# Performance work log

Measured on AMD Instinct MI355X. Metric: run time of the kernel, lower is better.

The kernel has to match this reference:

```python
import jax, jax.numpy as jnp
import numpy as np
import math

B, S, D, H, DFF = 4, 1024, 1024, 16, 4096
DK = D // H
EPS = 1e-5


def setup_inputs() -> dict:
    key = jax.random.key(0)
    ks = jax.random.split(key, 16)
    sc = 0.02
    inp = {
        "x": jax.random.normal(ks[0], (B, S, D), jnp.float32),
        "Wq": jax.random.normal(ks[1], (D, D), jnp.float32) * sc,
        "bq": jnp.zeros((D,), jnp.float32),
        "Wk": jax.random.normal(ks[2], (D, D), jnp.float32) * sc,
        "bk": jnp.zeros((D,), jnp.float32),
        "Wv": jax.random.normal(ks[3], (D, D), jnp.float32) * sc,
        "bv": jnp.zeros((D,), jnp.float32),
        "Wo": jax.random.normal(ks[4], (D, D), jnp.float32) * sc,
        "bo": jnp.zeros((D,), jnp.float32),
        "W1": jax.random.normal(ks[5], (D, DFF), jnp.float32) * sc,
        "b1": jnp.zeros((DFF,), jnp.float32),
        "W2": jax.random.normal(ks[6], (DFF, D), jnp.float32) * sc,
        "b2": jnp.zeros((D,), jnp.float32),
        "g1": jnp.ones((D,), jnp.float32),
        "be1": jnp.zeros((D,), jnp.float32),
        "g2": jnp.ones((D,), jnp.float32),
        "be2": jnp.zeros((D,), jnp.float32),
    }
    return inp


def _layernorm(x, g, b):
    mu = jnp.mean(x, axis=-1, keepdims=True)
    var = jnp.mean(jnp.square(x - mu), axis=-1, keepdims=True)
    return (x - mu) * jax.lax.rsqrt(var + EPS) * g + b


def reference(x, Wq, bq, Wk, bk, Wv, bv, Wo, bo, W1, b1, W2, b2, g1, be1, g2, be2):
    # multi-head self-attention (dropout = identity, eval mode)
    q = (x @ Wq + bq).reshape(B, S, H, DK).transpose(0, 2, 1, 3)  # [B,H,S,DK]
    k = (x @ Wk + bk).reshape(B, S, H, DK).transpose(0, 2, 1, 3)
    v = (x @ Wv + bv).reshape(B, S, H, DK).transpose(0, 2, 1, 3)
    scores = jnp.einsum("bhqd,bhkd->bhqk", q, k) / math.sqrt(DK)
    attn_weights = jax.nn.softmax(scores, axis=-1)
    ctx = jnp.einsum("bhqk,bhkd->bhqd", attn_weights, v)
    ctx = ctx.transpose(0, 2, 1, 3).reshape(B, S, D)
    attn_out = ctx @ Wo + bo
    x = _layernorm(x + attn_out, g1, be1)
    ff = jax.nn.relu(x @ W1 + b1) @ W2 + b2
    x = _layernorm(x + ff, g2, be2)
    return x, attn_weights
```

## Files before the change

### kernel.cpp

```cpp
#include <hip/hip_runtime.h>

typedef unsigned short u16;
typedef __attribute__((ext_vector_type(8))) short bf16x8;
typedef __attribute__((ext_vector_type(4))) float f32x4;

__device__ __forceinline__ u16 f2b(float f) {
  unsigned u = __float_as_uint(f);
  u += 0x7fffu + ((u >> 16) & 1u);
  return (u16)(u >> 16);
}
__device__ __forceinline__ float b2f(u16 v) {
  return __uint_as_float((unsigned)v << 16);
}

__device__ __forceinline__ void gload16(const u16* g, u16* l) {
  __builtin_amdgcn_global_load_lds((__attribute__((address_space(1))) void*)(g),
                                   (__attribute__((address_space(3))) void*)(l), 16, 0, 0);
}

__global__ __launch_bounds__(256) void cast_k(const float* __restrict__ s,
                                              u16* __restrict__ d, int n4) {
  int i = blockIdx.x * 256 + threadIdx.x;
  if (i >= n4) return;
  float4 v = *(const float4*)(s + (size_t)i * 4);
  ushort4 o = make_ushort4(f2b(v.x), f2b(v.y), f2b(v.z), f2b(v.w));
  *(ushort4*)(d + (size_t)i * 4) = o;
}

__global__ __launch_bounds__(256) void transpose_k(const float* __restrict__ src,
                                                   u16* __restrict__ dst,
                                                   int ldsrc, int lddst) {
  __shared__ float t[32][33];
  int c0 = blockIdx.x * 32, r0 = blockIdx.y * 32;
  int tx = threadIdx.x, ty = threadIdx.y;
#pragma unroll
  for (int i = 0; i < 4; ++i)
    t[ty + i * 8][tx] = src[(size_t)(r0 + ty + i * 8) * ldsrc + c0 + tx];
  __syncthreads();
#pragma unroll
  for (int i = 0; i < 4; ++i)
    dst[(size_t)(c0 + ty + i * 8) * lddst + r0 + tx] = f2b(t[tx][ty + i * 8]);
}

__global__ __launch_bounds__(256) void transpose_v_k(const u16* __restrict__ qkv,
                                                     u16* __restrict__ vt) {
  __shared__ u16 t[32][33];
  int z = blockIdx.z;
  int b = z >> 4, h = z & 15;
  int s0 = blockIdx.x * 32, d0 = blockIdx.y * 32;
  int tx = threadIdx.x, ty = threadIdx.y;
  const u16* src = qkv + (size_t)(b * 1024) * 3072 + 2048 + h * 64;
  u16* dst = vt + (size_t)z * 65536;
#pragma unroll
  for (int i = 0; i < 4; ++i)
    t[ty + i * 8][tx] = src[(size_t)(s0 + ty + i * 8) * 3072 + d0 + tx];
  __syncthreads();
#pragma unroll
  for (int i = 0; i < 4; ++i)
    dst[(size_t)(d0 + ty + i * 8) * 1024 + s0 + tx] = t[tx][ty + i * 8];
}

template <int BN, int BIAS, int RELU, int EXPE, int RSCALE, int SB16, int SF32>
__global__ __launch_bounds__(256) void gemm_k(
    const u16* __restrict__ Ab, long aHi, long aLo, int lda,
    const u16* __restrict__ Bt, long bHi, long bLo, int ldb,
    float* __restrict__ Cf, u16* __restrict__ Cb,
    long cHi, long cLo, int ldc,
    const float* __restrict__ bias, const float* __restrict__ rs,
    int K, int ZD) {
  constexpr int NT = BN / 32;
  constexpr int CB = (BN * 64 * 2) / 1024;
  __shared__ __align__(128) u16 As[128 * 64];
  __shared__ __align__(128) u16 Bs[BN * 64];

  const int tid = threadIdx.x;
  const int lane = tid & 63;
  const int wave = tid >> 6;
  const int waveM = wave >> 1, waveN = wave & 1;
  const int quad = lane >> 4, l16 = lane & 15;

  const int zb = blockIdx.z / ZD, zr = blockIdx.z % ZD;
  const long aOff = zb * aHi + zr * aLo;
  const long bOff = zb * bHi + zr * bLo;
  const long cOff = zb * cHi + zr * cLo;

  const int row0 = blockIdx.y * 128;
  const int col0 = blockIdx.x * BN;

  const int lr = lane >> 3;
  const int lc = (lane & 7) * 8;

  f32x4 acc[4][NT] = {};

  for (int k0 = 0; k0 < K; k0 += 64) {
    const u16* Ag = Ab + aOff + (long)row0 * lda + k0;
    const u16* Bg = Bt + bOff + (long)col0 * ldb + k0;
#pragma unroll
    for (int c = 0; c < 4; ++c) {
      int ch = c * 4 + wave;
      gload16(Ag + (long)(ch * 8 + lr) * lda + lc, &As[ch * 512]);
    }
#pragma unroll
    for (int c = 0; c < CB / 4; ++c) {
      int ch = c * 4 + wave;
      gload16(Bg + (long)(ch * 8 + lr) * ldb + lc, &Bs[ch * 512]);
    }
    __syncthreads();

    bf16x8 af[4][2], bfr[NT][2];
#pragma unroll
    for (int mi = 0; mi < 4; ++mi)
#pragma unroll
      for (int ks = 0; ks < 2; ++ks)
        af[mi][ks] = *(const bf16x8*)&As[(waveM * 64 + mi * 16 + l16) * 64 + ks * 32 + quad * 8];
#pragma unroll
    for (int ni = 0; ni < NT; ++ni)
#pragma unroll
      for (int ks = 0; ks < 2; ++ks)
        bfr[ni][ks] = *(const bf16x8*)&Bs[(waveN * (BN / 2) + ni * 16 + l16) * 64 + ks * 32 + quad * 8];
#pragma unroll
    for (int ks = 0; ks < 2; ++ks)
#pragma unroll
      for (int mi = 0; mi < 4; ++mi)
#pragma unroll
        for (int ni = 0; ni < NT; ++ni)
          acc[mi][ni] = __builtin_amdgcn_mfma_f32_16x16x32_bf16(af[mi][ks], bfr[ni][ks], acc[mi][ni], 0, 0, 0);
    __syncthreads();
  }

#pragma unroll
  for (int ni = 0; ni < NT; ++ni) {
    int col = col0 + waveN * (BN / 2) + ni * 16 + l16;
    float bv = BIAS ? bias[col] : 0.f;
#pragma unroll
    for (int mi = 0; mi < 4; ++mi) {
#pragma unroll
      for (int r = 0; r < 4; ++r) {
        int row = row0 + waveM * 64 + mi * 16 + quad * 4 + r;
        float v = acc[mi][ni][r] + bv;
        if (RELU) v = fmaxf(v, 0.f);
        if (EXPE) v = __expf(v * 0.125f);
        if (RSCALE) v *= rs[(long)blockIdx.z * 1024 + row];
        long idx = cOff + (long)row * ldc + col;
        if (SF32) Cf[idx] = v;
        if (SB16) Cb[idx] = f2b(v);
      }
    }
  }
}

__global__ __launch_bounds__(256) void norm_k(const u16* __restrict__ e,
                                              float* __restrict__ w,
                                              float* __restrict__ inv) {
  long row = blockIdx.x;
  int tid = threadIdx.x;
  ushort4 ev = *(const ushort4*)(e + row * 1024 + tid * 4);
  float4 v;
  v.x = b2f(ev.x); v.y = b2f(ev.y); v.z = b2f(ev.z); v.w = b2f(ev.w);
  float s = v.x + v.y + v.z + v.w;
#pragma unroll
  for (int d = 32; d > 0; d >>= 1) s += __shfl_xor(s, d);
  __shared__ float red[4];
  if ((tid & 63) == 0) red[tid >> 6] = s;
  __syncthreads();
  s = red[0] + red[1] + red[2] + red[3];
  float r = 1.f / s;
  float4 o = make_float4(v.x * r, v.y * r, v.z * r, v.w * r);
  *(float4*)(w + row * 1024 + tid * 4) = o;
  if (tid == 0) inv[row] = r;
}

template <int WB16>
__global__ __launch_bounds__(256) void add_ln_k(const float* __restrict__ xp,
                                                const float* __restrict__ yp,
                                                const float* __restrict__ g,
                                                const float* __restrict__ bta,
                                                float* __restrict__ of,
                                                u16* __restrict__ ob) {
  long row = blockIdx.x;
  int tid = threadIdx.x;
  const float4 xv = *(const float4*)(xp + row * 1024 + tid * 4);
  const float4 yv = *(const float4*)(yp + row * 1024 + tid * 4);
  float4 v = make_float4(xv.x + yv.x, xv.y + yv.y, xv.z + yv.z, xv.w + yv.w);
  float s1 = v.x + v.y + v.z + v.w;
  float s2 = v.x * v.x + v.y * v.y + v.z * v.z + v.w * v.w;
#pragma unroll
  for (int d = 32; d > 0; d >>= 1) {
    s1 += __shfl_xor(s1, d);
    s2 += __shfl_xor(s2, d);
  }
  __shared__ float r1[4], r2[4];
  if ((tid & 63) == 0) { r1[tid >> 6] = s1; r2[tid >> 6] = s2; }
  __syncthreads();
  s1 = r1[0] + r1[1] + r1[2] + r1[3];
  s2 = r2[0] + r2[1] + r2[2] + r2[3];
  float mu = s1 * (1.f / 1024.f);
  float var = s2 * (1.f / 1024.f) - mu * mu;
  float rs = rsqrtf(var + 1e-5f);
  float4 gv = *(const float4*)(g + tid * 4);
  float4 bv = *(const float4*)(bta + tid * 4);
  float4 o;
  o.x = (v.x - mu) * rs * gv.x + bv.x;
  o.y = (v.y - mu) * rs * gv.y + bv.y;
  o.z = (v.z - mu) * rs * gv.z + bv.z;
  o.w = (v.w - mu) * rs * gv.w + bv.w;
  *(float4*)(of + row * 1024 + tid * 4) = o;
  if (WB16) {
    ushort4 ov = make_ushort4(f2b(o.x), f2b(o.y), f2b(o.z), f2b(o.w));
    *(ushort4*)(ob + row * 1024 + tid * 4) = ov;
  }
}

extern "C" void kernel_launch(void* const* d_in, const int* in_sizes, int n_in,
                              void* d_out, int out_size, void* d_ws, size_t ws_size,
                              hipStream_t stream) {
  const float* x   = (const float*)d_in[0];
  const float* Wq  = (const float*)d_in[1];
  const float* bq  = (const float*)d_in[2];
  const float* Wk  = (const float*)d_in[3];
  const float* bk  = (const float*)d_in[4];
  const float* Wv  = (const float*)d_in[5];
  const float* bv  = (const float*)d_in[6];
  const float* Wo  = (const float*)d_in[7];
  const float* bo  = (const float*)d_in[8];
  const float* W1  = (const float*)d_in[9];
  const float* b1  = (const float*)d_in[10];
  const float* W2  = (const float*)d_in[11];
  const float* b2  = (const float*)d_in[12];
  const float* g1  = (const float*)d_in[13];
  const float* be1 = (const float*)d_in[14];
  const float* g2  = (const float*)d_in[15];
  const float* be2 = (const float*)d_in[16];

  float* out = (float*)d_out;
  float* attn = out + 4194304LL;

  char* w = (char*)d_ws;
  size_t off = 0;
  auto alloc = [&](size_t bytes) {
    void* p = w + off;
    off = (off + bytes + 255) & ~(size_t)255;
    return p;
  };
  u16* xb        = (u16*)alloc(8388608);
  u16* Wqkvt     = (u16*)alloc(6291456);
  u16* Wot       = (u16*)alloc(2097152);
  u16* W1t       = (u16*)alloc(8388608);
  u16* W2t       = (u16*)alloc(8388608);
  float* bqkv    = (float*)alloc(12288);
  u16* qkvb      = (u16*)alloc(25165824);
  u16* vtb       = (u16*)alloc(8388608);
  u16* expb      = (u16*)alloc(134217728);
  float* inv     = (float*)alloc(262144);
  u16* ctxb      = (u16*)alloc(8388608);
  float* attn_o  = (float*)alloc(16777216);
  float* x1      = (float*)alloc(16777216);
  u16* x1b       = (u16*)alloc(8388608);
  u16* ff1b      = (u16*)alloc(33554432);
  float* ff2     = (float*)alloc(16777216);
  (void)ws_size; (void)in_sizes; (void)n_in; (void)out_size;

  dim3 tb(32, 8);
  cast_k<<<4096, 256, 0, stream>>>(x, xb, 1048576);
  transpose_k<<<dim3(32, 32), tb, 0, stream>>>(Wq, Wqkvt,           1024, 1024);
  transpose_k<<<dim3(32, 32), tb, 0, stream>>>(Wk, Wqkvt + 1048576, 1024, 1024);
  transpose_k<<<dim3(32, 32), tb, 0, stream>>>(Wv, Wqkvt + 2097152, 1024, 1024);
  transpose_k<<<dim3(32, 32), tb, 0, stream>>>(Wo, Wot, 1024, 1024);
  transpose_k<<<dim3(128, 32), tb, 0, stream>>>(W1, W1t, 4096, 1024);
  transpose_k<<<dim3(32, 128), tb, 0, stream>>>(W2, W2t, 1024, 4096);
  hipMemcpyAsync(bqkv,        bq, 4096, hipMemcpyDeviceToDevice, stream);
  hipMemcpyAsync(bqkv + 1024, bk, 4096, hipMemcpyDeviceToDevice, stream);
  hipMemcpyAsync(bqkv + 2048, bv, 4096, hipMemcpyDeviceToDevice, stream);

  gemm_k<128, 1, 0, 0, 0, 1, 0><<<dim3(24, 32, 1), 256, 0, stream>>>(
      xb, 0, 0, 1024, Wqkvt, 0, 0, 1024,
      nullptr, qkvb, 0, 0, 3072, bqkv, nullptr, 1024, 1);

  transpose_v_k<<<dim3(32, 2, 64), tb, 0, stream>>>(qkvb, vtb);

  gemm_k<128, 0, 0, 1, 0, 1, 0><<<dim3(8, 8, 64), 256, 0, stream>>>(
      qkvb, 3145728L, 64, 3072,
      qkvb + 1024, 3145728L, 64, 3072,
      nullptr, expb, 16777216L, 1048576L, 1024, nullptr, nullptr, 64, 16);

  norm_k<<<65536, 256, 0, stream>>>(expb, attn, inv);

  gemm_k<64, 0, 0, 0, 1, 1, 0><<<dim3(1, 8, 64), 256, 0, stream>>>(
      expb, 16777216L, 1048576L, 1024,
      vtb, 1048576L, 65536L, 1024,
      nullptr, ctxb, 1048576L, 64, 1024, nullptr, inv, 1024, 16);

  gemm_k<128, 1, 0, 0, 0, 0, 1><<<dim3(8, 32, 1), 256, 0, stream>>>(
      ctxb, 0, 0, 1024, Wot, 0, 0, 1024,
      attn_o, nullptr, 0, 0, 1024, bo, nullptr, 1024, 1);

  add_ln_k<1><<<4096, 256, 0, stream>>>(x, attn_o, g1, be1, x1, x1b);

  gemm_k<128, 1, 1, 0, 0, 1, 0><<<dim3(32, 32, 1), 256, 0, stream>>>(
      x1b, 0, 0, 1024, W1t, 0, 0, 1024,
      nullptr, ff1b, 0, 0, 4096, b1, nullptr, 1024, 1);

  gemm_k<128, 1, 0, 0, 0, 0, 1><<<dim3(8, 32, 1), 256, 0, stream>>>(
      ff1b, 0, 0, 4096, W2t, 0, 0, 4096,
      ff2, nullptr, 0, 0, 1024, b2, nullptr, 4096, 1);

  add_ln_k<0><<<4096, 256, 0, stream>>>(x1, ff2, g2, be2, out, nullptr);
}
```

Measured before the change: 753.9 us.

## Fuse score GEMM with softmax, fold residual into GEMM epilogue, merge weight transposes

Replaces the score GEMM, separate bf16 exp write, and row-normalization kernel with one kernel. It computes QK^T per 64-row tile, keeps exp values in registers, reduces the row sums and writes normalized fp32 attention plus bf16 probabilities. This removes a full re-read of the 128MB exp buffer. The residual add moves into the Wo and W2 GEMM epilogues, and those GEMMs switch to BN=64 with more blocks. The four square weight transposes merge into one launch, and the bias memcpys are replaced by multi-pointer bias selection. The fused softmax holds 128 packed registers per thread, which limits occupancy and risks spills.

```diff
diff --git a/kernel.cpp b/kernel.cpp
--- a/kernel.cpp
+++ b/kernel.cpp
@@ -40,6 +40,27 @@
 #pragma unroll
   for (int i = 0; i < 4; ++i)
     dst[(size_t)(c0 + ty + i * 8) * lddst + r0 + tx] = f2b(t[tx][ty + i * 8]);
+}
+
+__global__ __launch_bounds__(256) void transpose4_k(const float* __restrict__ Wq,
+                                                    const float* __restrict__ Wk,
+                                                    const float* __restrict__ Wv,
+                                                    const float* __restrict__ Wo,
+                                                    u16* __restrict__ Wqkvt,
+                                                    u16* __restrict__ Wot) {
+  __shared__ float t[32][33];
+  int z = blockIdx.z;
+  const float* src = z == 0 ? Wq : z == 1 ? Wk : z == 2 ? Wv : Wo;
+  u16* dst = z < 3 ? Wqkvt + (size_t)z * 1048576 : Wot;
+  int c0 = blockIdx.x * 32, r0 = blockIdx.y * 32;
+  int tx = threadIdx.x, ty = threadIdx.y;
+#pragma unroll
+  for (int i = 0; i < 4; ++i)
+    t[ty + i * 8][tx] = src[(size_t)(r0 + ty + i * 8) * 1024 + c0 + tx];
+  __syncthreads();
+#pragma unroll
+  for (int i = 0; i < 4; ++i)
+    dst[(size_t)(c0 + ty + i * 8) * 1024 + r0 + tx] = f2b(t[tx][ty + i * 8]);
 }
 
 __global__ __launch_bounds__(256) void transpose_v_k(const u16* __restrict__ qkv,
@@ -57,16 +78,17 @@
   __syncthreads();
 #pragma unroll
   for (int i = 0; i < 4; ++i)
-    dst[(size_t)(d0 + ty + i * 8) * 1024 + s0 + tx] = t[tx][ty + i * 8];
-}
-
-template <int BN, int BIAS, int RELU, int EXPE, int RSCALE, int SB16, int SF32>
+    dst[(size_t)(d0 + i * 8 + ty) * 1024 + s0 + tx] = t[tx][ty + i * 8];
+}
+
+template <int BN, int BIAS, int RELU, int SB16, int SF32, int RESID>
 __global__ __launch_bounds__(256) void gemm_k(
     const u16* __restrict__ Ab, long aHi, long aLo, int lda,
     const u16* __restrict__ Bt, long bHi, long bLo, int ldb,
     float* __restrict__ Cf, u16* __restrict__ Cb,
     long cHi, long cLo, int ldc,
-    const float* __restrict__ bias, const float* __restrict__ rs,
+    const float* __restrict__ bias, const float* __restrict__ biasB,
+    const float* __restrict__ biasC, const float* __restrict__ resid,
     int K, int ZD) {
   constexpr int NT = BN / 32;
   constexpr int CB = (BN * 64 * 2) / 1024;
@@ -131,7 +153,9 @@
 #pragma unroll
   for (int ni = 0; ni < NT; ++ni) {
     int col = col0 + waveN * (BN / 2) + ni * 16 + l16;
-    float bv = BIAS ? bias[col] : 0.f;
+    float bv = 0.f;
+    if (BIAS == 1) bv = bias[col];
+    if (BIAS == 3) bv = col < 1024 ? bias[col] : (col < 2048 ? biasB[col - 1024] : biasC[col - 2048]);
 #pragma unroll
     for (int mi = 0; mi < 4; ++mi) {
 #pragma unroll
@@ -139,9 +163,8 @@
         int row = row0 + waveM * 64 + mi * 16 + quad * 4 + r;
         float v = acc[mi][ni][r] + bv;
         if (RELU) v = fmaxf(v, 0.f);
-        if (EXPE) v = __expf(v * 0.125f);
-        if (RSCALE) v *= rs[(long)blockIdx.z * 1024 + row];
         long idx = cOff + (long)row * ldc + col;
+        if (RESID) v += resid[idx];
         if (SF32) Cf[idx] = v;
         if (SB16) Cb[idx] = f2b(v);
       }
@@ -149,28 +172,87 @@
   }
 }
 
-__global__ __launch_bounds__(256) void norm_k(const u16* __restrict__ e,
-                                              float* __restrict__ w,
-                                              float* __restrict__ inv) {
-  long row = blockIdx.x;
-  int tid = threadIdx.x;
-  ushort4 ev = *(const ushort4*)(e + row * 1024 + tid * 4);
-  float4 v;
-  v.x = b2f(ev.x); v.y = b2f(ev.y); v.z = b2f(ev.z); v.w = b2f(ev.w);
-  float s = v.x + v.y + v.z + v.w;
-#pragma unroll
-  for (int d = 32; d > 0; d >>= 1) s += __shfl_xor(s, d);
-  __shared__ float red[4];
-  if ((tid & 63) == 0) red[tid >> 6] = s;
-  __syncthreads();
-  s = red[0] + red[1] + red[2] + red[3];
-  float r = 1.f / s;
-  float4 o = make_float4(v.x * r, v.y * r, v.z * r, v.w * r);
-  *(float4*)(w + row * 1024 + tid * 4) = o;
-  if (tid == 0) inv[row] = r;
-}
-
-template <int WB16>
+__global__ __launch_bounds__(256) void score_softmax_k(const u16* __restrict__ qkvb,
+                                                       float* __restrict__ attn,
+                                                       u16* __restrict__ expb) {
+  __shared__ __align__(128) u16 Bs[256 * 64];
+  const int tid = threadIdx.x;
+  const int lane = tid & 63;
+  const int w = tid >> 6;
+  const int quad = lane >> 4, l16 = lane & 15;
+  const int lr = lane >> 3, lc = (lane & 7) * 8;
+
+  const int z = blockIdx.y;
+  const int b = z >> 4, h = z & 15;
+  const u16* Q  = qkvb + (long)b * 3145728 + h * 64;
+  const u16* Kt = qkvb + (long)b * 3145728 + 1024 + h * 64;
+
+  const int qrow = blockIdx.x * 64 + w * 16 + l16;
+  bf16x8 af[2];
+  af[0] = *(const bf16x8*)&Q[(long)qrow * 3072 + quad * 8];
+  af[1] = *(const bf16x8*)&Q[(long)qrow * 3072 + 32 + quad * 8];
+
+  unsigned p[4][32];
+  float rowpart[4] = {0.f, 0.f, 0.f, 0.f};
+
+#pragma unroll 4
+  for (int nc = 0; nc < 4; ++nc) {
+#pragma unroll
+    for (int c = 0; c < 8; ++c) {
+      int ch = c * 4 + w;
+      gload16(Kt + (long)(nc * 256 + ch * 8 + lr) * 3072 + lc, &Bs[ch * 512]);
+    }
+    __syncthreads();
+#pragma unroll
+    for (int ni = 0; ni < 16; ++ni) {
+      bf16x8 b0 = *(const bf16x8*)&Bs[(ni * 16 + l16) * 64 + quad * 8];
+      bf16x8 b1 = *(const bf16x8*)&Bs[(ni * 16 + l16) * 64 + 32 + quad * 8];
+      f32x4 acc = {};
+      acc = __builtin_amdgcn_mfma_f32_16x16x32_bf16(af[0], b0, acc, 0, 0, 0);
+      acc = __builtin_amdgcn_mfma_f32_16x16x32_bf16(af[1], b1, acc, 0, 0, 0);
+      float e0 = __expf(acc[0] * 0.125f);
+      float e1 = __expf(acc[1] * 0.125f);
+      float e2 = __expf(acc[2] * 0.125f);
+      float e3 = __expf(acc[3] * 0.125f);
+      rowpart[0] += e0; rowpart[1] += e1; rowpart[2] += e2; rowpart[3] += e3;
+      p[nc][ni * 2]     = (unsigned)f2b(e0) | ((unsigned)f2b(e1) << 16);
+      p[nc][ni * 2 + 1] = (unsigned)f2b(e2) | ((unsigned)f2b(e3) << 16);
+    }
+    __syncthreads();
+  }
+
+#pragma unroll
+  for (int d = 1; d < 16; d <<= 1) {
+#pragma unroll
+    for (int r = 0; r < 4; ++r) rowpart[r] += __shfl_xor(rowpart[r], d);
+  }
+  float inv0 = 1.f / rowpart[0], inv1 = 1.f / rowpart[1];
+  float inv2 = 1.f / rowpart[2], inv3 = 1.f / rowpart[3];
+
+  const long rbase = (long)z * 1048576 + (long)(blockIdx.x * 64 + w * 16 + quad * 4) * 1024;
+#pragma unroll 4
+  for (int nc = 0; nc < 4; ++nc) {
+#pragma unroll
+    for (int ni = 0; ni < 16; ++ni) {
+      int col = nc * 256 + ni * 16 + l16;
+      unsigned w0 = p[nc][ni * 2], w1 = p[nc][ni * 2 + 1];
+      float e0 = b2f((u16)(w0 & 0xffff)) * inv0;
+      float e1 = b2f((u16)(w0 >> 16)) * inv1;
+      float e2 = b2f((u16)(w1 & 0xffff)) * inv2;
+      float e3 = b2f((u16)(w1 >> 16)) * inv3;
+      attn[rbase + col] = e0;
+      attn[rbase + 1024 + col] = e1;
+      attn[rbase + 2048 + col] = e2;
+      attn[rbase + 3072 + col] = e3;
+      expb[rbase + col] = f2b(e0);
+      expb[rbase + 1024 + col] = f2b(e1);
+      expb[rbase + 2048 + col] = f2b(e2);
+      expb[rbase + 3072 + col] = f2b(e3);
+    }
+  }
+}
+
+template <int WB16, int ADD>
 __global__ __launch_bounds__(256) void add_ln_k(const float* __restrict__ xp,
                                                 const float* __restrict__ yp,
                                                 const float* __restrict__ g,
@@ -179,9 +261,11 @@
                                                 u16* __restrict__ ob) {
   long row = blockIdx.x;
   int tid = threadIdx.x;
-  const float4 xv = *(const float4*)(xp + row * 1024 + tid * 4);
-  const float4 yv = *(const float4*)(yp + row * 1024 + tid * 4);
-  float4 v = make_float4(xv.x + yv.x, xv.y + yv.y, xv.z + yv.z, xv.w + yv.w);
+  float4 v = *(const float4*)(xp + row * 1024 + tid * 4);
+  if (ADD) {
+    const float4 yv = *(const float4*)(yp + row * 1024 + tid * 4);
+    v.x += yv.x; v.y += yv.y; v.z += yv.z; v.w += yv.w;
+  }
   float s1 = v.x + v.y + v.z + v.w;
   float s2 = v.x * v.x + v.y * v.y + v.z * v.z + v.w * v.w;
 #pragma unroll
@@ -247,11 +331,9 @@
   u16* Wot       = (u16*)alloc(2097152);
   u16* W1t       = (u16*)alloc(8388608);
   u16* W2t       = (u16*)alloc(8388608);
-  float* bqkv    = (float*)alloc(12288);
   u16* qkvb      = (u16*)alloc(25165824);
   u16* vtb       = (u16*)alloc(8388608);
   u16* expb      = (u16*)alloc(134217728);
-  float* inv     = (float*)alloc(262144);
   u16* ctxb      = (u16*)alloc(8388608);
   float* attn_o  = (float*)alloc(16777216);
   float* x1      = (float*)alloc(16777216);
@@ -262,47 +344,36 @@
 
   dim3 tb(32, 8);
   cast_k<<<4096, 256, 0, stream>>>(x, xb, 1048576);
-  transpose_k<<<dim3(32, 32), tb, 0, stream>>>(Wq, Wqkvt,           1024, 1024);
-  transpose_k<<<dim3(32, 32), tb, 0, stream>>>(Wk, Wqkvt + 1048576, 1024, 1024);
-  transpose_k<<<dim3(32, 32), tb, 0, stream>>>(Wv, Wqkvt + 2097152, 1024, 1024);
-  transpose_k<<<dim3(32, 32), tb, 0, stream>>>(Wo, Wot, 1024, 1024);
+  transpose4_k<<<dim3(32, 32, 4), tb, 0, stream>>>(Wq, Wk, Wv, Wo, Wqkvt, Wot);
   transpose_k<<<dim3(128, 32), tb, 0, stream>>>(W1, W1t, 4096, 1024);
   transpose_k<<<dim3(32, 128), tb, 0, stream>>>(W2, W2t, 1024, 4096);
-  hipMemcpyAsync(bqkv,        bq, 4096, hipMemcpyDeviceToDevice, stream);
-  hipMemcpyAsync(bqkv + 1024, bk, 4096, hipMemcpyDeviceToDevice, stream);
-  hipMemcpyAsync(bqkv + 2048, bv, 4096, hipMemcpyDeviceToDevice, stream);
-
-  gemm_k<128, 1, 0, 0, 0, 1, 0><<<dim3(24, 32, 1), 256, 0, stream>>>(
+
+  gemm_k<128, 3, 0, 1, 0, 0><<<dim3(24, 32, 1), 256, 0, stream>>>(
       xb, 0, 0, 1024, Wqkvt, 0, 0, 1024,
-      nullptr, qkvb, 0, 0, 3072, bqkv, nullptr, 1024, 1);
+      nullptr, qkvb, 0, 0, 3072, bq, bk, bv, nullptr, 1024, 1);
 
   transpose_v_k<<<dim3(32, 2, 64), tb, 0, stream>>>(qkvb, vtb);
 
-  gemm_k<128, 0, 0, 1, 0, 1, 0><<<dim3(8, 8, 64), 256, 0, stream>>>(
-      qkvb, 3145728L, 64, 3072,
-      qkvb + 1024, 3145728L, 64, 3072,
-      nullptr, expb, 16777216L, 1048576L, 1024, nullptr, nullptr, 64, 16);
-
-  norm_k<<<65536, 256, 0, stream>>>(expb, attn, inv);
-
-  gemm_k<64, 0, 0, 0, 1, 1, 0><<<dim3(1, 8, 64), 256, 0, stream>>>(
+  score_softmax_k<<<dim3(16, 64), 256, 0, stream>>>(qkvb, attn, expb);
+
+  gemm_k<64, 0, 0, 1, 0, 0><<<dim3(1, 8, 64), 256, 0, stream>>>(
       expb, 16777216L, 1048576L, 1024,
       vtb, 1048576L, 65536L, 1024,
-      nullptr, ctxb, 1048576L, 64, 1024, nullptr, inv, 1024, 16);
-
-  gemm_k<128, 1, 0, 0, 0, 0, 1><<<dim3(8, 32, 1), 256, 0, stream>>>(
+      nullptr, ctxb, 1048576L, 64, 1024, nullptr, nullptr, nullptr, nullptr, 1024, 16);
+
+  gemm_k<64, 1, 0, 0, 1, 1><<<dim3(16, 32, 1), 256, 0, stream>>>(
       ctxb, 0, 0, 1024, Wot, 0, 0, 1024,
-      attn_o, nullptr, 0, 0, 1024, bo, nullptr, 1024, 1);
-
-  add_ln_k<1><<<4096, 256, 0, stream>>>(x, attn_o, g1, be1, x1, x1b);
-
-  gemm_k<128, 1, 1, 0, 0, 1, 0><<<dim3(32, 32, 1), 256, 0, stream>>>(
+      attn_o, nullptr, 0, 0, 1024, bo, nullptr, nullptr, x, 1024, 1);
+
+  add_ln_k<1, 0><<<4096, 256, 0, stream>>>(attn_o, nullptr, g1, be1, x1, x1b);
+
+  gemm_k<128, 1, 1, 1, 0, 0><<<dim3(32, 32, 1), 256, 0, stream>>>(
       x1b, 0, 0, 1024, W1t, 0, 0, 1024,
-      nullptr, ff1b, 0, 0, 4096, b1, nullptr, 1024, 1);
-
-  gemm_k<128, 1, 0, 0, 0, 0, 1><<<dim3(8, 32, 1), 256, 0, stream>>>(
+      nullptr, ff1b, 0, 0, 4096, b1, nullptr, nullptr, nullptr, 1024, 1);
+
+  gemm_k<64, 1, 0, 0, 1, 1><<<dim3(16, 32, 1), 256, 0, stream>>>(
       ff1b, 0, 0, 4096, W2t, 0, 0, 4096,
-      ff2, nullptr, 0, 0, 1024, b2, nullptr, 4096, 1);
-
-  add_ln_k<0><<<4096, 256, 0, stream>>>(x1, ff2, g2, be2, out, nullptr);
-}
+      ff2, nullptr, 0, 0, 1024, b2, nullptr, nullptr, x1, 4096, 1);
+
+  add_ln_k<0, 0><<<4096, 256, 0, stream>>>(ff2, nullptr, g2, be2, out, nullptr);
+}
```

New measurement: 727.0 us. 3.6% less time.
